# Optimization experiments

Measured on AMD Instinct MI355X. Metric: run time of the kernel, lower is better.

## Reference

```python
import jax, jax.numpy as jnp
import numpy as np

N_NODES = 100000
N_EDGES = 1600000
IN_C, HID_C, OUT_C = 128, 128, 40
BN_EPS = 1e-5


def gcn_conv(x, W, b, edge_index, n):
    # PyG GCNConv: h = x @ W, add self-loops, symmetric normalization, scatter-add to targets, + bias
    h = x @ W  # [N, C_out]
    loops = jnp.arange(n, dtype=edge_index.dtype)
    src = jnp.concatenate([edge_index[0], loops])  # messages flow source -> target
    dst = jnp.concatenate([edge_index[1], loops])
    deg = jax.ops.segment_sum(jnp.ones_like(dst, dtype=h.dtype), dst, num_segments=n)
    dinv = jnp.where(deg > 0, jax.lax.rsqrt(deg), 0.0).astype(h.dtype)
    norm = dinv[src] * dinv[dst]  # [E+N]
    msg = h[src] * norm[:, None]
    out = jax.ops.segment_sum(msg, dst, num_segments=n)
    return out + b


def batch_norm(x, gamma, beta):
    # training-mode batchnorm over the node dimension (biased variance, as torch)
    mean = jnp.mean(x, axis=0)
    var = jnp.mean(jnp.square(x - mean), axis=0)
    return (x - mean) * jax.lax.rsqrt(var + BN_EPS) * gamma + beta


def setup_inputs() -> dict:
    key = jax.random.key(0)
    ks = jax.random.split(key, 8)
    x = jax.random.normal(ks[0], (N_NODES, IN_C), dtype=jnp.float32)
    edge_index = jax.random.randint(ks[1], (2, N_EDGES), 0, N_NODES, dtype=jnp.int64)
    def glorot(k, fi, fo):
        s = np.sqrt(6.0 / (fi + fo)).astype(np.float32)
        return jax.random.uniform(k, (fi, fo), jnp.float32, -s, s)
    return {
        "x": x,
        "edge_index": edge_index,
        "W1": glorot(ks[2], IN_C, HID_C), "b1": jnp.zeros((HID_C,), jnp.float32),
        "g1": jnp.ones((HID_C,), jnp.float32), "bt1": jnp.zeros((HID_C,), jnp.float32),
        "W2": glorot(ks[3], HID_C, HID_C), "b2": jnp.zeros((HID_C,), jnp.float32),
        "g2": jnp.ones((HID_C,), jnp.float32), "bt2": jnp.zeros((HID_C,), jnp.float32),
        "W3": glorot(ks[4], HID_C, OUT_C), "b3": jnp.zeros((OUT_C,), jnp.float32),
    }


def reference(x, edge_index, W1, b1, g1, bt1, W2, b2, g2, bt2, W3, b3):
    n = x.shape[0]
    # layer 1: GCNConv -> BatchNorm -> ReLU (dropout p=0.0 / eval -> identity)
    h = gcn_conv(x, W1, b1, edge_index, n)
    h = jax.nn.relu(batch_norm(h, g1, bt1))
    # layer 2
    h = gcn_conv(h, W2, b2, edge_index, n)
    h = jax.nn.relu(batch_norm(h, g2, bt2))
    # output layer (no norm/act)
    return gcn_conv(h, W3, b3, edge_index, n)
```

## Files before the change

kernel.cpp:

```cpp
#include <hip/hip_runtime.h>
#include <hip/hip_fp16.h>
#include <cstdint>

#define BN_EPS 1e-5f
#define PCHUNK 4096
#define BCAP 16384

typedef _Float16 f16;
typedef _Float16 f16x8 __attribute__((ext_vector_type(8)));
typedef _Float16 f16x4 __attribute__((ext_vector_type(4)));
typedef float f32x4 __attribute__((ext_vector_type(4)));


__global__ void detect_k(const unsigned* __restrict__ eb, int E,
                         int* __restrict__ flag) {
  int t = threadIdx.x;
  int cov = min(2048, E);
  int nz = 0;
  for (int k = t; k < cov; k += 256) nz |= (eb[2 * k + 1] != 0u);
  if (nz) atomicOr(flag, 1);
}

__device__ __forceinline__ void load_edge(const void* eb, int E, bool w64,
                                          int e, int& s, int& d) {
  if (w64) {
    const long long* p = (const long long*)eb;
    s = (int)p[e];
    d = (int)p[E + e];
  } else {
    const int* p = (const int*)eb;
    s = p[e];
    d = p[E + e];
  }
}

__global__ __launch_bounds__(256) void part_k(const void* __restrict__ eb, int E,
                                              const int* __restrict__ flag,
                                              int* __restrict__ realtot,
                                              int* __restrict__ pcur,
                                              int2* __restrict__ part) {
  __shared__ int hist[256], lofs[256], gbase[256], lcur[256];
  __shared__ int sa[256], sb[256];
  __shared__ int2 stage[PCHUNK];
  bool w64 = (*flag == 0);
  const int t = threadIdx.x;
  const int e0 = blockIdx.x * PCHUNK;
  const int cnt = min(PCHUNK, E - e0);
  hist[t] = 0;
  __syncthreads();
  int2 ed[16];
#pragma unroll
  for (int k = 0; k < 16; k++) {
    int idx = t + k * 256;
    if (idx < cnt) {
      int s, d;
      load_edge(eb, E, w64, e0 + idx, s, d);
      ed[k].x = s;
      ed[k].y = d;
      atomicAdd(&hist[d >> 9], 1);
    }
  }
  __syncthreads();
  sa[t] = hist[t];
  __syncthreads();
  int* src = sa;
  int* dst = sb;
  for (int off = 1; off < 256; off <<= 1) {
    int val = src[t] + (t >= off ? src[t - off] : 0);
    dst[t] = val;
    __syncthreads();
    int* tmp = src; src = dst; dst = tmp;
  }
  int c = hist[t];
  lofs[t] = src[t] - c;
  int cpad = (c + 7) & ~7;
  gbase[t] = (c > 0) ? (t * BCAP + atomicAdd(&pcur[t], cpad)) : 0;
  if (c > 0) atomicAdd(&realtot[t], c);
  lcur[t] = src[t] - c;
  __syncthreads();
#pragma unroll
  for (int k = 0; k < 16; k++) {
    int idx = t + k * 256;
    if (idx < cnt) {
      int b = ed[k].y >> 9;
      int p = atomicAdd(&lcur[b], 1);
      stage[p] = ed[k];
    }
  }
  __syncthreads();
  for (int idx = t; idx < cnt; idx += 256) {
    int2 e = stage[idx];
    int b = e.y >> 9;
    part[gbase[b] + (idx - lofs[b])] = e;
  }
  if (c > 0) {
    for (int k = c; k < cpad; k++) part[gbase[t] + k] = make_int2(0, -1);
  }
}

__global__ void bscan_k(const int* __restrict__ realtot, int* __restrict__ rbase,
                        int* __restrict__ rp, int nbkt, int n, int E) {
  __shared__ int sa[256], sb[256];
  int t = threadIdx.x;
  int v = (t < nbkt) ? realtot[t] : 0;
  sa[t] = v;
  __syncthreads();
  int* src = sa;
  int* dst = sb;
  for (int off = 1; off < 256; off <<= 1) {
    int val = src[t] + (t >= off ? src[t - off] : 0);
    dst[t] = val;
    __syncthreads();
    int* tmp = src; src = dst; dst = tmp;
  }
  rbase[t] = src[t] - v;
  if (t == 0) rp[n] = E;
}

__global__ __launch_bounds__(512) void sort_k(const int2* __restrict__ part,
                                              const int* __restrict__ pcur,
                                              const int* __restrict__ rbase,
                                              int* __restrict__ rp,
                                              float* __restrict__ dinv,
                                              int* __restrict__ csr, int n) {
  __shared__ int lhist[512], lcur[512];
  __shared__ int sa[512], sb[512];
  const int b = blockIdx.x;
  const int d0 = b << 9;
  const int t = threadIdx.x;
  const int nloc = min(512, n - d0);
  lhist[t] = 0;
  __syncthreads();
  const int base = b * BCAP;
  const int T = pcur[b];
  for (int idx = t; idx < T; idx += 512) {
    int2 e = part[base + idx];
    if (e.y >= 0) atomicAdd(&lhist[e.y - d0], 1);
  }
  __syncthreads();
  sa[t] = lhist[t];
  __syncthreads();
  int* src = sa;
  int* dst = sb;
  for (int off = 1; off < 512; off <<= 1) {
    int val = src[t] + (t >= off ? src[t - off] : 0);
    dst[t] = val;
    __syncthreads();
    int* tmp = src; src = dst; dst = tmp;
  }
  int c = lhist[t];
  int gpos = rbase[b] + src[t] - c;
  if (t < nloc) {
    rp[d0 + t] = gpos;
    dinv[d0 + t] = rsqrtf((float)(c + 1));
  }
  lcur[t] = gpos;
  __syncthreads();
  for (int idx = t; idx < T; idx += 512) {
    int2 e = part[base + idx];
    if (e.y >= 0) {
      int pos = atomicAdd(&lcur[e.y - d0], 1);
      csr[pos] = e.x;
    }
  }
}

__global__ void prep_all(const float* __restrict__ W1, const float* __restrict__ W2,
                         const float* __restrict__ W3, f16* __restrict__ Wt1,
                         f16* __restrict__ Wt2, f16* __restrict__ Wt3) {
  int b = blockIdx.x, k = threadIdx.x;
  if (b < 128) {
    Wt1[(size_t)b * 128 + k] = (f16)W1[(size_t)k * 128 + b];
  } else if (b < 256) {
    int nc = b - 128;
    Wt2[(size_t)nc * 128 + k] = (f16)W2[(size_t)k * 128 + nc];
  } else {
    int nc = b - 256;
    Wt3[(size_t)nc * 128 + k] = (nc < 40) ? (f16)W3[(size_t)k * 40 + nc] : (f16)0.f;
  }
}

template <int NCP, bool BN, bool F32IN>
__global__ __launch_bounds__(256) void gemm_mfma(const void* __restrict__ Xv,
                                                 const f16* __restrict__ Wt,
                                                 const float* __restrict__ bn_acc,
                                                 const float* __restrict__ g,
                                                 const float* __restrict__ bt,
                                                 float inv_n,
                                                 const float* __restrict__ dinv,
                                                 f16* __restrict__ H, int n) {
  constexpr int CB = NCP / 16;
  __shared__ f16 Xs[128][136];
  __shared__ f16 Ws[NCP][136];
  __shared__ float bnS[128], bnH[128];
  const int t = threadIdx.x;
  const int m0 = blockIdx.x * 128;

  if (BN) {
    if (t < 128) {
      float mean = bn_acc[t] * inv_n;
      float var = bn_acc[128 + t] * inv_n - mean * mean;
      float sc = g[t] * rsqrtf(var + BN_EPS);
      bnS[t] = sc;
      bnH[t] = fmaf(-mean, sc, bt[t]);
    }
    __syncthreads();
  }

  if constexpr (F32IN) {
    const float* X = (const float*)Xv;
#pragma unroll
    for (int p = 0; p < 16; p++) {
      int idx = p * 256 + t;
      int row = idx >> 5, c = (idx & 31) * 4;
      float4 v = make_float4(0.f, 0.f, 0.f, 0.f);
      if (m0 + row < n) v = *(const float4*)&X[(size_t)(m0 + row) * 128 + c];
      if (BN) {
        v.x = fmaxf(fmaf(v.x, bnS[c + 0], bnH[c + 0]), 0.f);
        v.y = fmaxf(fmaf(v.y, bnS[c + 1], bnH[c + 1]), 0.f);
        v.z = fmaxf(fmaf(v.z, bnS[c + 2], bnH[c + 2]), 0.f);
        v.w = fmaxf(fmaf(v.w, bnS[c + 3], bnH[c + 3]), 0.f);
      }
      f16x4 h = {(f16)v.x, (f16)v.y, (f16)v.z, (f16)v.w};
      *(f16x4*)&Xs[row][c] = h;
    }
  } else {
    const f16* X = (const f16*)Xv;
#pragma unroll
    for (int p = 0; p < 8; p++) {
      int idx = p * 256 + t;
      int row = idx >> 4, c = (idx & 15) * 8;
      f16x8 v = {0, 0, 0, 0, 0, 0, 0, 0};
      if (m0 + row < n) v = *(const f16x8*)&X[(size_t)(m0 + row) * 128 + c];
      if (BN) {
#pragma unroll
        for (int j = 0; j < 8; j++) {
          float f = (float)v[j];
          f = fmaxf(fmaf(f, bnS[c + j], bnH[c + j]), 0.f);
          v[j] = (f16)f;
        }
      }
      *(f16x8*)&Xs[row][c] = v;
    }
  }
#pragma unroll
  for (int idx = t; idx < NCP * 16; idx += 256) {
    int row = idx >> 4, c = (idx & 15) * 8;
    *(f16x8*)&Ws[row][c] = *(const f16x8*)&Wt[(size_t)row * 128 + c];
  }
  __syncthreads();

  const int w = t >> 6, l = t & 63;
  const int lr = l & 15, lq = l >> 4;
  f32x4 acc[2][CB];
#pragma unroll
  for (int i = 0; i < 2; i++)
#pragma unroll
    for (int j = 0; j < CB; j++) acc[i][j] = (f32x4){0.f, 0.f, 0.f, 0.f};

#pragma unroll
  for (int kb = 0; kb < 4; kb++) {
    f16x8 xf0 = *(const f16x8*)&Xs[w * 32 + lr][kb * 32 + lq * 8];
    f16x8 xf1 = *(const f16x8*)&Xs[w * 32 + 16 + lr][kb * 32 + lq * 8];
#pragma unroll
    for (int cb = 0; cb < CB; cb++) {
      f16x8 wf = *(const f16x8*)&Ws[cb * 16 + lr][kb * 32 + lq * 8];
      acc[0][cb] = __builtin_amdgcn_mfma_f32_16x16x32_f16(wf, xf0, acc[0][cb], 0, 0, 0);
      acc[1][cb] = __builtin_amdgcn_mfma_f32_16x16x32_f16(wf, xf1, acc[1][cb], 0, 0, 0);
    }
  }
#pragma unroll
  for (int rg = 0; rg < 2; rg++) {
    int row = m0 + w * 32 + rg * 16 + lr;
    if (row >= n) continue;
    float dv = dinv[row];
#pragma unroll
    for (int cb = 0; cb < CB; cb++) {
      int col = cb * 16 + lq * 4;
      f32x4 a = acc[rg][cb];
      f16x4 h = {(f16)(a[0] * dv), (f16)(a[1] * dv), (f16)(a[2] * dv),
                 (f16)(a[3] * dv)};
      *(f16x4*)&H[(size_t)row * NCP + col] = h;
    }
  }
}

__global__ __launch_bounds__(256) void agg128h(const f16* __restrict__ H,
                                               const int* __restrict__ rp,
                                               const int* __restrict__ csr,
                                               const float* __restrict__ dinv,
                                               const float* __restrict__ bias,
                                               f16* __restrict__ out, int n) {
  const int lane = threadIdx.x & 63;
  const int hl = lane & 31, side = lane >> 5;
  const int gw = (blockIdx.x * 256 + threadIdx.x) >> 6;
  const int nw = (gridDim.x * 256) >> 6;
  const int npairs = (n + 1) >> 1;
  const float4 bs = *(const float4*)&bias[hl * 4];
  for (int p = gw; p < npairs; p += nw) {
    const int i = p * 2 + side;
    const bool valid = (i < n);
    const int ic = valid ? i : 0;
    f16x4 hv = *(const f16x4*)&H[(size_t)ic * 128 + hl * 4];
    float a0 = (float)hv[0];
    float a1 = (float)hv[1];
    float a2 = (float)hv[2];
    float a3 = (float)hv[3];
    int e0 = rp[ic];
    int cnt = valid ? (rp[ic + 1] - e0) : 0;
    int maxc = max(cnt, __shfl_xor(cnt, 32));
    int j = 0;
    for (; j + 8 <= maxc; j += 8) {
      int xs[8], ss[8];
      float ww[8];
#pragma unroll
      for (int k = 0; k < 8; k++) xs[k] = (j + k < cnt) ? e0 + j + k : 0;
#pragma unroll
      for (int k = 0; k < 8; k++) ss[k] = csr[xs[k]];
#pragma unroll
      for (int k = 0; k < 8; k++) ww[k] = (j + k < cnt) ? 1.f : 0.f;
      f16x4 vv[8];
#pragma unroll
      for (int k = 0; k < 8; k++)
        vv[k] = *(const f16x4*)&H[(size_t)ss[k] * 128 + hl * 4];
#pragma unroll
      for (int k = 0; k < 8; k++) {
        a0 = fmaf((float)vv[k][0], ww[k], a0);
        a1 = fmaf((float)vv[k][1], ww[k], a1);
        a2 = fmaf((float)vv[k][2], ww[k], a2);
        a3 = fmaf((float)vv[k][3], ww[k], a3);
      }
    }
    for (; j < maxc; j++) {
      int x0 = (j < cnt) ? e0 + j : 0;
      int s0 = csr[x0];
      float w0 = (j < cnt) ? 1.f : 0.f;
      f16x4 v0 = *(const f16x4*)&H[(size_t)s0 * 128 + hl * 4];
      a0 = fmaf((float)v0[0], w0, a0); a1 = fmaf((float)v0[1], w0, a1);
      a2 = fmaf((float)v0[2], w0, a2); a3 = fmaf((float)v0[3], w0, a3);
    }
    if (valid) {
      float dv = dinv[ic];
      f16x4 h = {(f16)fmaf(a0, dv, bs.x), (f16)fmaf(a1, dv, bs.y),
                 (f16)fmaf(a2, dv, bs.z), (f16)fmaf(a3, dv, bs.w)};
      *(f16x4*)&out[(size_t)i * 128 + hl * 4] = h;
    }
  }
}

__global__ __launch_bounds__(256) void agg64h(const f16* __restrict__ H,
                                              const int* __restrict__ rp,
                                              const int* __restrict__ csr,
                                              const float* __restrict__ dinv,
                                              const float* __restrict__ bias,
                                              float* __restrict__ out, int n) {
  const int lane = threadIdx.x & 63;
  const int hl = lane & 31, side = lane >> 5;
  const int gw = (blockIdx.x * 256 + threadIdx.x) >> 6;
  const int nw = (gridDim.x * 256) >> 6;
  const int npairs = (n + 1) >> 1;
  const int col0 = hl * 2, col1 = hl * 2 + 1;
  const float b0 = (col0 < 40) ? bias[col0] : 0.f;
  const float b1 = (col1 < 40) ? bias[col1] : 0.f;
  for (int p = gw; p < npairs; p += nw) {
    const int i = p * 2 + side;
    const bool valid = (i < n);
    const int ic = valid ? i : 0;
    float2 hf = __half22float2(*(const __half2*)&H[(size_t)ic * 64 + col0]);
    float a0 = hf.x;
    float a1 = hf.y;
    int e0 = rp[ic];
    int cnt = valid ? (rp[ic + 1] - e0) : 0;
    int maxc = max(cnt, __shfl_xor(cnt, 32));
    int j = 0;
    for (; j + 8 <= maxc; j += 8) {
      int xs[8], ss[8];
      float ww[8];
#pragma unroll
      for (int k = 0; k < 8; k++) xs[k] = (j + k < cnt) ? e0 + j + k : 0;
#pragma unroll
      for (int k = 0; k < 8; k++) ss[k] = csr[xs[k]];
#pragma unroll
      for (int k = 0; k < 8; k++) ww[k] = (j + k < cnt) ? 1.f : 0.f;
      float2 vv[8];
#pragma unroll
      for (int k = 0; k < 8; k++)
        vv[k] = __half22float2(*(const __half2*)&H[(size_t)ss[k] * 64 + col0]);
#pragma unroll
      for (int k = 0; k < 8; k++) {
        a0 = fmaf(vv[k].x, ww[k], a0);
        a1 = fmaf(vv[k].y, ww[k], a1);
      }
    }
    for (; j < maxc; j++) {
      int x0 = (j < cnt) ? e0 + j : 0;
      int s0 = csr[x0];
      float w0 = (j < cnt) ? 1.f : 0.f;
      float2 v0 = __half22float2(*(const __half2*)&H[(size_t)s0 * 64 + col0]);
      a0 = fmaf(v0.x, w0, a0);
      a1 = fmaf(v0.y, w0, a1);
    }
    if (valid) {
      float dv = dinv[ic];
      if (col0 < 40) out[(size_t)i * 40 + col0] = fmaf(a0, dv, b0);
      if (col1 < 40) out[(size_t)i * 40 + col1] = fmaf(a1, dv, b1);
    }
  }
}

__global__ __launch_bounds__(256) void bn_stats_h(const f16* __restrict__ H, int n,
                                                  float* __restrict__ acc) {
  int t = threadIdx.x;
  int c2 = t & 63;
  int rg = t >> 6;
  float2 s = {0.f, 0.f}, s2 = {0.f, 0.f};
  for (int r = blockIdx.x * 4 + rg; r < n; r += gridDim.x * 4) {
    float2 v = __half22float2(*(const __half2*)&H[(size_t)r * 128 + c2 * 2]);
    s.x += v.x;
    s.y += v.y;
    s2.x = fmaf(v.x, v.x, s2.x);
    s2.y = fmaf(v.y, v.y, s2.y);
  }
  __shared__ float ls[4][128], ls2[4][128];
  ls[rg][c2 * 2] = s.x;
  ls[rg][c2 * 2 + 1] = s.y;
  ls2[rg][c2 * 2] = s2.x;
  ls2[rg][c2 * 2 + 1] = s2.y;
  __syncthreads();
  if (t < 128) {
    float a_ = ls[0][t] + ls[1][t] + ls[2][t] + ls[3][t];
    float b_ = ls2[0][t] + ls2[1][t] + ls2[2][t] + ls2[3][t];
    atomicAdd(&acc[t], a_);
    atomicAdd(&acc[128 + t], b_);
  }
}

extern "C" void kernel_launch(void* const* d_in, const int* in_sizes, int n_in,
                              void* d_out, int out_size, void* d_ws, size_t ws_size,
                              hipStream_t stream) {
  const float* x = (const float*)d_in[0];
  const void* eb = d_in[1];
  const float* W1 = (const float*)d_in[2];
  const float* b1 = (const float*)d_in[3];
  const float* g1 = (const float*)d_in[4];
  const float* bt1 = (const float*)d_in[5];
  const float* W2 = (const float*)d_in[6];
  const float* b2 = (const float*)d_in[7];
  const float* g2 = (const float*)d_in[8];
  const float* bt2 = (const float*)d_in[9];
  const float* W3 = (const float*)d_in[10];
  const float* b3 = (const float*)d_in[11];

  const int n = in_sizes[0] / 128;
  const int E = in_sizes[1] / 2;
  const float inv_n = 1.0f / (float)n;

  char* w = (char*)d_ws;
  auto alloc = [&](size_t bytes) {
    void* p = (void*)w;
    w += (bytes + 255) & ~(size_t)255;
    return p;
  };
  const int NBKT = (n + 511) / 512;
  f16* hA = (f16*)alloc((size_t)n * 128 * 2);
  f16* hB = (f16*)alloc((size_t)n * 128 * 2);
  int* csr = (int*)alloc((size_t)E * 4);
  int2* part = (int2*)alloc((size_t)NBKT * BCAP * 8);
  float* dinv = (float*)alloc((size_t)n * 4);
  int* rp = (int*)alloc((size_t)(n + 1) * 4);
  int* rbase = (int*)alloc(256 * 4);
  f16* Wt1 = (f16*)alloc(128 * 128 * 2);
  f16* Wt2 = (f16*)alloc(128 * 128 * 2);
  f16* Wt3 = (f16*)alloc(64 * 128 * 2);
  int* pcur = (int*)alloc(256 * 4);
  int* realtot = (int*)alloc(256 * 4);
  float* bn_acc1 = (float*)alloc(256 * 4);
  float* bn_acc2 = (float*)alloc(256 * 4);
  int* flag = (int*)alloc(256);
  size_t zbytes = (char*)flag + 256 - (char*)pcur;
  hipMemsetAsync(pcur, 0, zbytes, stream);

  const int PB = (E + PCHUNK - 1) / PCHUNK;

  prep_all<<<320, 128, 0, stream>>>(W1, W2, W3, Wt1, Wt2, Wt3);

  detect_k<<<1, 256, 0, stream>>>((const unsigned*)eb, E, flag);
  part_k<<<PB, 256, 0, stream>>>(eb, E, flag, realtot, pcur, part);
  bscan_k<<<1, 256, 0, stream>>>(realtot, rbase, rp, NBKT, n, E);
  sort_k<<<NBKT, 512, 0, stream>>>(part, pcur, rbase, rp, dinv, csr, n);

  const int GB = (n + 127) / 128;
  const int AGB = 4096;

  gemm_mfma<128, false, true><<<GB, 256, 0, stream>>>(x, Wt1, nullptr, nullptr,
                                                      nullptr, inv_n, dinv, hA, n);
  agg128h<<<AGB, 256, 0, stream>>>(hA, rp, csr, dinv, b1, hB, n);
  bn_stats_h<<<1024, 256, 0, stream>>>(hB, n, bn_acc1);
  gemm_mfma<128, true, false><<<GB, 256, 0, stream>>>(hB, Wt2, bn_acc1, g1, bt1,
                                                      inv_n, dinv, hA, n);
  agg128h<<<AGB, 256, 0, stream>>>(hA, rp, csr, dinv, b2, hB, n);
  bn_stats_h<<<1024, 256, 0, stream>>>(hB, n, bn_acc2);
  gemm_mfma<64, true, false><<<GB, 256, 0, stream>>>(hB, Wt3, bn_acc2, g2, bt2,
                                                     inv_n, dinv, hA, n);
  agg64h<<<AGB, 256, 0, stream>>>(hA, rp, csr, dinv, b3, (float*)d_out, n);
}
```

Before: 461.0 us.

## Fold index-width detect and bucket scan into neighbours; widen aggregation lanes

Removes the separate detect_k and bscan_k launches. The index-width check moves into each part_k block, which samples its own chunk, and each sort_k block recomputes its bucket base with a shared-memory reduction over realtot. The aggregation kernels now let each wavefront handle four nodes with 16 lanes each and wider f16x8 and f16x4 gathers, which halves the lanes per row and makes loads and stores wider. In exchange, lane utilisation can drop when degrees differ across the four nodes, and the per-block width detection could disagree between blocks on unusual inputs.

```diff
diff --git a/kernel.cpp b/kernel.cpp
--- a/kernel.cpp
+++ b/kernel.cpp
@@ -11,15 +11,6 @@
 typedef _Float16 f16x4 __attribute__((ext_vector_type(4)));
 typedef float f32x4 __attribute__((ext_vector_type(4)));
 
-
-__global__ void detect_k(const unsigned* __restrict__ eb, int E,
-                         int* __restrict__ flag) {
-  int t = threadIdx.x;
-  int cov = min(2048, E);
-  int nz = 0;
-  for (int k = t; k < cov; k += 256) nz |= (eb[2 * k + 1] != 0u);
-  if (nz) atomicOr(flag, 1);
-}
 
 __device__ __forceinline__ void load_edge(const void* eb, int E, bool w64,
                                           int e, int& s, int& d) {
@@ -35,19 +26,28 @@
 }
 
 __global__ __launch_bounds__(256) void part_k(const void* __restrict__ eb, int E,
-                                              const int* __restrict__ flag,
                                               int* __restrict__ realtot,
                                               int* __restrict__ pcur,
                                               int2* __restrict__ part) {
   __shared__ int hist[256], lofs[256], gbase[256], lcur[256];
   __shared__ int sa[256], sb[256];
   __shared__ int2 stage[PCHUNK];
-  bool w64 = (*flag == 0);
+  __shared__ int w64f;
   const int t = threadIdx.x;
   const int e0 = blockIdx.x * PCHUNK;
   const int cnt = min(PCHUNK, E - e0);
   hist[t] = 0;
-  __syncthreads();
+  if (t == 0) w64f = 0;
+  __syncthreads();
+  {
+    const unsigned* w = (const unsigned*)eb;
+    int nz = 0;
+    int cov = min(cnt, 512);
+    for (int k = t; k < cov; k += 256) nz |= (w[2 * (size_t)(e0 + k) + 1] != 0u);
+    if (nz) atomicOr(&w64f, 1);
+  }
+  __syncthreads();
+  const bool w64 = (w64f == 0);
   int2 ed[16];
 #pragma unroll
   for (int k = 0; k < 16; k++) {
@@ -98,37 +98,30 @@
   }
 }
 
-__global__ void bscan_k(const int* __restrict__ realtot, int* __restrict__ rbase,
-                        int* __restrict__ rp, int nbkt, int n, int E) {
-  __shared__ int sa[256], sb[256];
-  int t = threadIdx.x;
-  int v = (t < nbkt) ? realtot[t] : 0;
-  sa[t] = v;
-  __syncthreads();
-  int* src = sa;
-  int* dst = sb;
-  for (int off = 1; off < 256; off <<= 1) {
-    int val = src[t] + (t >= off ? src[t - off] : 0);
-    dst[t] = val;
-    __syncthreads();
-    int* tmp = src; src = dst; dst = tmp;
-  }
-  rbase[t] = src[t] - v;
-  if (t == 0) rp[n] = E;
-}
-
 __global__ __launch_bounds__(512) void sort_k(const int2* __restrict__ part,
                                               const int* __restrict__ pcur,
-                                              const int* __restrict__ rbase,
+                                              const int* __restrict__ realtot,
                                               int* __restrict__ rp,
                                               float* __restrict__ dinv,
-                                              int* __restrict__ csr, int n) {
+                                              int* __restrict__ csr, int n, int E,
+                                              int nbkt) {
   __shared__ int lhist[512], lcur[512];
   __shared__ int sa[512], sb[512];
   const int b = blockIdx.x;
   const int d0 = b << 9;
   const int t = threadIdx.x;
   const int nloc = min(512, n - d0);
+  int pacc = 0;
+  for (int j = t; j < b; j += 512) pacc += realtot[j];
+  sa[t] = pacc;
+  __syncthreads();
+  for (int off = 256; off > 0; off >>= 1) {
+    if (t < off) sa[t] += sa[t + off];
+    __syncthreads();
+  }
+  const int rbase = sa[0];
+  __syncthreads();
+
   lhist[t] = 0;
   __syncthreads();
   const int base = b * BCAP;
@@ -149,12 +142,13 @@
     int* tmp = src; src = dst; dst = tmp;
   }
   int c = lhist[t];
-  int gpos = rbase[b] + src[t] - c;
+  int gpos = rbase + src[t] - c;
   if (t < nloc) {
     rp[d0 + t] = gpos;
     dinv[d0 + t] = rsqrtf((float)(c + 1));
   }
   lcur[t] = gpos;
+  if (b == nbkt - 1 && t == 0) rp[n] = E;
   __syncthreads();
   for (int idx = t; idx < T; idx += 512) {
     int2 e = part[base + idx];
@@ -292,58 +286,60 @@
                                                const float* __restrict__ bias,
                                                f16* __restrict__ out, int n) {
   const int lane = threadIdx.x & 63;
-  const int hl = lane & 31, side = lane >> 5;
+  const int sub = lane >> 4;
+  const int cl = lane & 15;
   const int gw = (blockIdx.x * 256 + threadIdx.x) >> 6;
   const int nw = (gridDim.x * 256) >> 6;
-  const int npairs = (n + 1) >> 1;
-  const float4 bs = *(const float4*)&bias[hl * 4];
-  for (int p = gw; p < npairs; p += nw) {
-    const int i = p * 2 + side;
+  const int nquads = (n + 3) >> 2;
+  for (int q = gw; q < nquads; q += nw) {
+    const int i = q * 4 + sub;
     const bool valid = (i < n);
     const int ic = valid ? i : 0;
-    f16x4 hv = *(const f16x4*)&H[(size_t)ic * 128 + hl * 4];
-    float a0 = (float)hv[0];
-    float a1 = (float)hv[1];
-    float a2 = (float)hv[2];
-    float a3 = (float)hv[3];
+    f16x8 hv = *(const f16x8*)&H[(size_t)ic * 128 + cl * 8];
+    float a[8];
+#pragma unroll
+    for (int c = 0; c < 8; c++) a[c] = (float)hv[c];
     int e0 = rp[ic];
     int cnt = valid ? (rp[ic + 1] - e0) : 0;
-    int maxc = max(cnt, __shfl_xor(cnt, 32));
+    int m = max(cnt, __shfl_xor(cnt, 16));
+    m = max(m, __shfl_xor(m, 32));
     int j = 0;
-    for (; j + 8 <= maxc; j += 8) {
-      int xs[8], ss[8];
-      float ww[8];
-#pragma unroll
-      for (int k = 0; k < 8; k++) xs[k] = (j + k < cnt) ? e0 + j + k : 0;
-#pragma unroll
-      for (int k = 0; k < 8; k++) ss[k] = csr[xs[k]];
-#pragma unroll
-      for (int k = 0; k < 8; k++) ww[k] = (j + k < cnt) ? 1.f : 0.f;
-      f16x4 vv[8];
+    for (; j + 8 <= m; j += 8) {
+      int ss[8];
+#pragma unroll
+      for (int k = 0; k < 8; k++) ss[k] = csr[(j + k < cnt) ? e0 + j + k : 0];
+      f16x8 vv[8];
 #pragma unroll
       for (int k = 0; k < 8; k++)
-        vv[k] = *(const f16x4*)&H[(size_t)ss[k] * 128 + hl * 4];
+        vv[k] = *(const f16x8*)&H[(size_t)ss[k] * 128 + cl * 8];
 #pragma unroll
       for (int k = 0; k < 8; k++) {
-        a0 = fmaf((float)vv[k][0], ww[k], a0);
-        a1 = fmaf((float)vv[k][1], ww[k], a1);
-        a2 = fmaf((float)vv[k][2], ww[k], a2);
-        a3 = fmaf((float)vv[k][3], ww[k], a3);
+        float wk = (j + k < cnt) ? 1.f : 0.f;
+#pragma unroll
+        for (int c = 0; c < 8; c++) a[c] = fmaf((float)vv[k][c], wk, a[c]);
       }
     }
-    for (; j < maxc; j++) {
-      int x0 = (j < cnt) ? e0 + j : 0;
-      int s0 = csr[x0];
-      float w0 = (j < cnt) ? 1.f : 0.f;
-      f16x4 v0 = *(const f16x4*)&H[(size_t)s0 * 128 + hl * 4];
-      a0 = fmaf((float)v0[0], w0, a0); a1 = fmaf((float)v0[1], w0, a1);
-      a2 = fmaf((float)v0[2], w0, a2); a3 = fmaf((float)v0[3], w0, a3);
+    for (; j < m; j++) {
+      int s0 = csr[(j < cnt) ? e0 + j : 0];
+      f16x8 v0 = *(const f16x8*)&H[(size_t)s0 * 128 + cl * 8];
+      float wk = (j < cnt) ? 1.f : 0.f;
+#pragma unroll
+      for (int c = 0; c < 8; c++) a[c] = fmaf((float)v0[c], wk, a[c]);
     }
     if (valid) {
       float dv = dinv[ic];
-      f16x4 h = {(f16)fmaf(a0, dv, bs.x), (f16)fmaf(a1, dv, bs.y),
-                 (f16)fmaf(a2, dv, bs.z), (f16)fmaf(a3, dv, bs.w)};
-      *(f16x4*)&out[(size_t)i * 128 + hl * 4] = h;
+      float4 b0 = *(const float4*)&bias[cl * 8];
+      float4 b1 = *(const float4*)&bias[cl * 8 + 4];
+      f16x8 h;
+      h[0] = (f16)fmaf(a[0], dv, b0.x);
+      h[1] = (f16)fmaf(a[1], dv, b0.y);
+      h[2] = (f16)fmaf(a[2], dv, b0.z);
+      h[3] = (f16)fmaf(a[3], dv, b0.w);
+      h[4] = (f16)fmaf(a[4], dv, b1.x);
+      h[5] = (f16)fmaf(a[5], dv, b1.y);
+      h[6] = (f16)fmaf(a[6], dv, b1.z);
+      h[7] = (f16)fmaf(a[7], dv, b1.w);
+      *(f16x8*)&out[(size_t)i * 128 + cl * 8] = h;
     }
   }
 }
@@ -355,55 +351,58 @@
                                               const float* __restrict__ bias,
                                               float* __restrict__ out, int n) {
   const int lane = threadIdx.x & 63;
-  const int hl = lane & 31, side = lane >> 5;
+  const int sub = lane >> 4;
+  const int cl = lane & 15;
   const int gw = (blockIdx.x * 256 + threadIdx.x) >> 6;
   const int nw = (gridDim.x * 256) >> 6;
-  const int npairs = (n + 1) >> 1;
-  const int col0 = hl * 2, col1 = hl * 2 + 1;
-  const float b0 = (col0 < 40) ? bias[col0] : 0.f;
-  const float b1 = (col1 < 40) ? bias[col1] : 0.f;
-  for (int p = gw; p < npairs; p += nw) {
-    const int i = p * 2 + side;
+  const int nquads = (n + 3) >> 2;
+  for (int q = gw; q < nquads; q += nw) {
+    const int i = q * 4 + sub;
     const bool valid = (i < n);
     const int ic = valid ? i : 0;
-    float2 hf = __half22float2(*(const __half2*)&H[(size_t)ic * 64 + col0]);
-    float a0 = hf.x;
-    float a1 = hf.y;
+    f16x4 hv = *(const f16x4*)&H[(size_t)ic * 64 + cl * 4];
+    float a0 = (float)hv[0], a1 = (float)hv[1], a2 = (float)hv[2],
+          a3 = (float)hv[3];
     int e0 = rp[ic];
     int cnt = valid ? (rp[ic + 1] - e0) : 0;
-    int maxc = max(cnt, __shfl_xor(cnt, 32));
+    int m = max(cnt, __shfl_xor(cnt, 16));
+    m = max(m, __shfl_xor(m, 32));
     int j = 0;
-    for (; j + 8 <= maxc; j += 8) {
-      int xs[8], ss[8];
-      float ww[8];
-#pragma unroll
-      for (int k = 0; k < 8; k++) xs[k] = (j + k < cnt) ? e0 + j + k : 0;
-#pragma unroll
-      for (int k = 0; k < 8; k++) ss[k] = csr[xs[k]];
-#pragma unroll
-      for (int k = 0; k < 8; k++) ww[k] = (j + k < cnt) ? 1.f : 0.f;
-      float2 vv[8];
+    for (; j + 8 <= m; j += 8) {
+      int ss[8];
+#pragma unroll
+      for (int k = 0; k < 8; k++) ss[k] = csr[(j + k < cnt) ? e0 + j + k : 0];
+      f16x4 vv[8];
 #pragma unroll
       for (int k = 0; k < 8; k++)
-        vv[k] = __half22float2(*(const __half2*)&H[(size_t)ss[k] * 64 + col0]);
+        vv[k] = *(const f16x4*)&H[(size_t)ss[k] * 64 + cl * 4];
 #pragma unroll
       for (int k = 0; k < 8; k++) {
-        a0 = fmaf(vv[k].x, ww[k], a0);
-        a1 = fmaf(vv[k].y, ww[k], a1);
+        float wk = (j + k < cnt) ? 1.f : 0.f;
+        a0 = fmaf((float)vv[k][0], wk, a0);
+        a1 = fmaf((float)vv[k][1], wk, a1);
+        a2 = fmaf((float)vv[k][2], wk, a2);
+        a3 = fmaf((float)vv[k][3], wk, a3);
       }
     }
-    for (; j < maxc; j++) {
-      int x0 = (j < cnt) ? e0 + j : 0;
-      int s0 = csr[x0];
-      float w0 = (j < cnt) ? 1.f : 0.f;
-      float2 v0 = __half22float2(*(const __half2*)&H[(size_t)s0 * 64 + col0]);
-      a0 = fmaf(v0.x, w0, a0);
-      a1 = fmaf(v0.y, w0, a1);
-    }
-    if (valid) {
+    for (; j < m; j++) {
+      int s0 = csr[(j < cnt) ? e0 + j : 0];
+      f16x4 v0 = *(const f16x4*)&H[(size_t)s0 * 64 + cl * 4];
+      float wk = (j < cnt) ? 1.f : 0.f;
+      a0 = fmaf((float)v0[0], wk, a0);
+      a1 = fmaf((float)v0[1], wk, a1);
+      a2 = fmaf((float)v0[2], wk, a2);
+      a3 = fmaf((float)v0[3], wk, a3);
+    }
+    if (valid && cl < 10) {
       float dv = dinv[ic];
-      if (col0 < 40) out[(size_t)i * 40 + col0] = fmaf(a0, dv, b0);
-      if (col1 < 40) out[(size_t)i * 40 + col1] = fmaf(a1, dv, b1);
+      float4 bb = *(const float4*)&bias[cl * 4];
+      float4 o;
+      o.x = fmaf(a0, dv, bb.x);
+      o.y = fmaf(a1, dv, bb.y);
+      o.z = fmaf(a2, dv, bb.z);
+      o.w = fmaf(a3, dv, bb.w);
+      *(float4*)&out[(size_t)i * 40 + cl * 4] = o;
     }
   }
 }
@@ -468,7 +467,6 @@
   int2* part = (int2*)alloc((size_t)NBKT * BCAP * 8);
   float* dinv = (float*)alloc((size_t)n * 4);
   int* rp = (int*)alloc((size_t)(n + 1) * 4);
-  int* rbase = (int*)alloc(256 * 4);
   f16* Wt1 = (f16*)alloc(128 * 128 * 2);
   f16* Wt2 = (f16*)alloc(128 * 128 * 2);
   f16* Wt3 = (f16*)alloc(64 * 128 * 2);
@@ -476,18 +474,15 @@
   int* realtot = (int*)alloc(256 * 4);
   float* bn_acc1 = (float*)alloc(256 * 4);
   float* bn_acc2 = (float*)alloc(256 * 4);
-  int* flag = (int*)alloc(256);
-  size_t zbytes = (char*)flag + 256 - (char*)pcur;
+  size_t zbytes = (char*)bn_acc2 + 256 * 4 - (char*)pcur;
   hipMemsetAsync(pcur, 0, zbytes, stream);
 
   const int PB = (E + PCHUNK - 1) / PCHUNK;
 
   prep_all<<<320, 128, 0, stream>>>(W1, W2, W3, Wt1, Wt2, Wt3);
 
-  detect_k<<<1, 256, 0, stream>>>((const unsigned*)eb, E, flag);
-  part_k<<<PB, 256, 0, stream>>>(eb, E, flag, realtot, pcur, part);
-  bscan_k<<<1, 256, 0, stream>>>(realtot, rbase, rp, NBKT, n, E);
-  sort_k<<<NBKT, 512, 0, stream>>>(part, pcur, rbase, rp, dinv, csr, n);
+  part_k<<<PB, 256, 0, stream>>>(eb, E, realtot, pcur, part);
+  sort_k<<<NBKT, 512, 0, stream>>>(part, pcur, realtot, rp, dinv, csr, n, E, NBKT);
 
   const int GB = (n + 127) / 128;
   const int AGB = 4096;
```

Result: faster. 436.1 us (-5.4%).
